# Optimization experiments

Hardware: AMD Instinct MI355X
Metric: run time of the kernel (lower is better)

The kernel has to match this reference:

```python
import jax, jax.numpy as jnp
import numpy as np

N = 16384          # number of feature-bank patches
D_IN = 1024        # raw feature dim
D_PROJ = 128       # projection dim (dimension_to_project_features_to)
PERCENTAGE = 0.01
NUM_SAMPLES = int(N * PERCENTAGE)  # 163 greedy coreset iterations


def setup_inputs() -> dict:
    key = jax.random.key(0)
    k1, k2 = jax.random.split(key)
    features = jax.random.normal(k1, (N, D_IN), dtype=jnp.float32)
    # random linear projection (torch.nn.Linear(D_IN, D_PROJ, bias=False))
    W = jax.random.normal(k2, (D_IN, D_PROJ), dtype=jnp.float32) / np.sqrt(D_IN)
    return {"features": features, "W": W}


def reference(features, W):
    # _reduce_features: random linear projection to D_PROJ
    reduced = features @ W  # [N, D_PROJ]

    # _compute_batchwise_differences: pairwise Euclidean distances [N, N]
    sq = jnp.sum(reduced * reduced, axis=1)  # [N]
    dist2 = sq[:, None] + sq[None, :] - 2.0 * (reduced @ reduced.T)
    dist = jnp.sqrt(jnp.clip(dist2, 0.0, None))  # [N, N]

    # initial anchor distances: torch.norm(distance_matrix, dim=1)
    anchor0 = jnp.sqrt(jnp.sum(dist * dist, axis=1))  # [N]

    # greedy farthest-point sampling loop (fused via scan)
    def step(anchor, _):
        select_idx = jnp.argmax(anchor)
        col = jax.lax.dynamic_index_in_dim(dist.T, select_idx, axis=0,
                                           keepdims=False)  # dist[:, idx]
        anchor = jnp.minimum(anchor, col)
        return anchor, select_idx

    _, coreset_indices = jax.lax.scan(step, anchor0, None, length=NUM_SAMPLES)

    # return subsampled feature bank [NUM_SAMPLES, D_IN]
    return features[coreset_indices]
```

## Files before the change

### kernel.cpp

```cpp
#include <hip/hip_runtime.h>

#define NPTS 16384
#define DIN  1024
#define DP   128
#define NS   163
#define NBLK 64
#define BTHR 256
#define WPB  (BTHR / 64)

__global__ __launch_bounds__(256) void k_proj(const float* __restrict__ F,
                                              const float* __restrict__ W,
                                              float* __restrict__ R) {
    __shared__ float As[32][36];
    __shared__ float Bs[32][128];
    const int tid = threadIdx.x;
    const int bm  = blockIdx.x;
    const int lr  = tid >> 3;
    const int lc  = (tid & 7) * 4;
    const int bkr = tid >> 5;
    const int bc  = (tid & 31) * 4;
    const int r0  = (tid >> 5) * 4;
    const int c0  = (tid & 31) * 4;

    float acc[4][4] = {};

    for (int k0 = 0; k0 < DIN; k0 += 32) {
        __syncthreads();
        *(float4*)&As[lr][lc] =
            *(const float4*)&F[(size_t)(bm * 32 + lr) * DIN + k0 + lc];
        #pragma unroll
        for (int p = 0; p < 4; ++p) {
            const int kk = bkr + p * 8;
            *(float4*)&Bs[kk][bc] = *(const float4*)&W[(size_t)(k0 + kk) * DP + bc];
        }
        __syncthreads();
        #pragma unroll
        for (int kt = 0; kt < 32; kt += 4) {
            float4 a[4], b[4];
            #pragma unroll
            for (int i = 0; i < 4; ++i) a[i] = *(const float4*)&As[r0 + i][kt];
            #pragma unroll
            for (int j = 0; j < 4; ++j) b[j] = *(const float4*)&Bs[kt + j][c0];
            #pragma unroll
            for (int i = 0; i < 4; ++i) {
                acc[i][0] += a[i].x * b[0].x; acc[i][1] += a[i].x * b[0].y;
                acc[i][2] += a[i].x * b[0].z; acc[i][3] += a[i].x * b[0].w;
                acc[i][0] += a[i].y * b[1].x; acc[i][1] += a[i].y * b[1].y;
                acc[i][2] += a[i].y * b[1].z; acc[i][3] += a[i].y * b[1].w;
                acc[i][0] += a[i].z * b[2].x; acc[i][1] += a[i].z * b[2].y;
                acc[i][2] += a[i].z * b[2].z; acc[i][3] += a[i].z * b[2].w;
                acc[i][0] += a[i].w * b[3].x; acc[i][1] += a[i].w * b[3].y;
                acc[i][2] += a[i].w * b[3].z; acc[i][3] += a[i].w * b[3].w;
            }
        }
    }
    #pragma unroll
    for (int i = 0; i < 4; ++i) {
        float4 v = make_float4(acc[i][0], acc[i][1], acc[i][2], acc[i][3]);
        *(float4*)&R[(size_t)(bm * 32 + r0 + i) * DP + c0] = v;
    }
}

__global__ void k_sq(const float* __restrict__ R, float* __restrict__ sq) {
    const int lane = threadIdx.x & 63;
    const int wave = (blockIdx.x * blockDim.x + threadIdx.x) >> 6;
    for (int row = wave; row < NPTS; row += 256) {
        const float a = R[(size_t)row * DP + lane];
        const float b = R[(size_t)row * DP + 64 + lane];
        float v = a * a + b * b;
        #pragma unroll
        for (int off = 32; off; off >>= 1) v += __shfl_xor(v, off);
        if (lane == 0) sq[row] = v;
    }
}

__global__ __launch_bounds__(256) void k_colpart(const float* __restrict__ R,
                                                 const float* __restrict__ sq,
                                                 float* __restrict__ part,
                                                 float* __restrict__ part_sq,
                                                 unsigned long long* __restrict__ gmax) {
    const int b = blockIdx.x, tid = threadIdx.x;

    const int slot = b * 256 + tid;
    if (slot < NS * NBLK) gmax[slot] = 0ull;

    if (tid < DP) {
        float acc = 0.0f;
        const float* p = R + (size_t)b * 256 * DP + tid;
        #pragma unroll 8
        for (int r = 0; r < 256; ++r) acc += p[(size_t)r * DP];
        part[b * DP + tid] = acc;
    } else if (tid < 192) {
        const int lane = tid - 128;
        const float* s = sq + b * 256;
        float v = s[lane] + s[64 + lane] + s[128 + lane] + s[192 + lane];
        #pragma unroll
        for (int off = 32; off; off >>= 1) v += __shfl_xor(v, off);
        if (lane == 0) part_sq[b] = v;
    }
}

__global__ void k_colfin(const float* __restrict__ part, const float* __restrict__ part_sq,
                         float* __restrict__ tS) {
    const int tid = threadIdx.x;
    if (tid < DP) {
        float acc = 0.0f;
        #pragma unroll 8
        for (int b = 0; b < 64; ++b) acc += part[b * DP + tid];
        tS[tid] = acc;
    } else if (tid == DP) {
        float s = 0.0f;
        #pragma unroll
        for (int b = 0; b < 64; ++b) s += part_sq[b];
        tS[DP] = s;
    }
}

__global__ __launch_bounds__(BTHR, 1) void k_greedy(
    const float* __restrict__ R, const float* __restrict__ sq,
    const float* __restrict__ tS, const float* __restrict__ F,
    unsigned long long* gmax, float* __restrict__ out) {
    __shared__ unsigned long long lmax[WPB];
    __shared__ unsigned sidx_cur;
    __shared__ unsigned sidx[(NS + NBLK - 1) / NBLK];

    const int tid  = threadIdx.x;
    const int lane = tid & 63;
    const int wid  = tid >> 6;
    const int bid  = blockIdx.x;
    const int g    = bid * BTHR + tid;

    float4 rr[32];
    #pragma unroll
    for (int q = 0; q < 32; ++q) rr[q] = *(const float4*)&R[(size_t)g * DP + q * 4];
    const float sqi = sq[g];

    float a0 = 0.f, a1 = 0.f, a2 = 0.f, a3 = 0.f;
    #pragma unroll
    for (int q = 0; q < 32; ++q) {
        const float4 t4 = *(const float4*)&tS[q * 4];
        a0 += rr[q].x * t4.x; a1 += rr[q].y * t4.y;
        a2 += rr[q].z * t4.z; a3 += rr[q].w * t4.w;
    }
    const float S = tS[DP];
    float anchor = sqrtf(fmaxf((float)NPTS * sqi + S - 2.0f * ((a0 + a1) + (a2 + a3)), 0.0f));

    for (int k = 0; k < NS; ++k) {
        unsigned long long key =
            ((unsigned long long)__float_as_uint(anchor) << 32) |
            (unsigned long long)(0xFFFFFFFFu - (unsigned)g);
        #pragma unroll
        for (int off = 32; off; off >>= 1) {
            const unsigned long long o = __shfl_xor(key, off);
            key = (o > key) ? o : key;
        }
        if (lane == 0) lmax[wid] = key;
        __syncthreads();

        if (wid == 0) {
            if (lane == 0) {
                unsigned long long bk = lmax[0];
                #pragma unroll
                for (int w = 1; w < WPB; ++w) bk = (lmax[w] > bk) ? lmax[w] : bk;
                __hip_atomic_store(&gmax[(size_t)k * NBLK + bid], bk,
                                   __ATOMIC_RELAXED, __HIP_MEMORY_SCOPE_AGENT);
            }
            const unsigned long long* gs = &gmax[(size_t)k * NBLK];
            unsigned long long v =
                __hip_atomic_load(&gs[lane], __ATOMIC_RELAXED, __HIP_MEMORY_SCOPE_AGENT);
            while (!__all(v != 0ull)) {
                __builtin_amdgcn_s_sleep(2);
                v = __hip_atomic_load(&gs[lane], __ATOMIC_RELAXED, __HIP_MEMORY_SCOPE_AGENT);
            }
            #pragma unroll
            for (int off = 32; off; off >>= 1) {
                const unsigned long long o = __shfl_xor(v, off);
                v = (o > v) ? o : v;
            }
            if (lane == 0) {
                const unsigned idx = 0xFFFFFFFFu - (unsigned)(v & 0xFFFFFFFFull);
                sidx_cur = idx;
                if ((k & 63) == bid) sidx[k >> 6] = idx;
            }
        }
        __syncthreads();
        const unsigned idx = sidx_cur;

        const float sqs = sq[idx];
        const float* rs = &R[(size_t)idx * DP];
        float d0 = 0.f, d1 = 0.f, d2 = 0.f, d3 = 0.f;
        #pragma unroll
        for (int q = 0; q < 32; ++q) {
            const float4 w4 = *(const float4*)&rs[q * 4];
            d0 += rr[q].x * w4.x; d1 += rr[q].y * w4.y;
            d2 += rr[q].z * w4.z; d3 += rr[q].w * w4.w;
        }
        const float d = sqrtf(fmaxf(sqi + sqs - 2.0f * ((d0 + d1) + (d2 + d3)), 0.0f));
        anchor = fminf(anchor, d);

        #pragma unroll
        for (int q = 0; q < 32; ++q)
            asm volatile("" : "+v"(rr[q].x), "+v"(rr[q].y), "+v"(rr[q].z), "+v"(rr[q].w));
    }

    __syncthreads();
    #pragma unroll
    for (int q = 0; q < 3; ++q) {
        const int k = q * NBLK + bid;
        if (k < NS) {
            const unsigned idx = sidx[q];
            *(float4*)&out[(size_t)k * DIN + tid * 4] =
                *(const float4*)&F[(size_t)idx * DIN + tid * 4];
        }
    }
}

extern "C" void kernel_launch(void* const* d_in, const int* in_sizes, int n_in,
                              void* d_out, int out_size, void* d_ws, size_t ws_size,
                              hipStream_t stream) {
    const float* F = (const float*)d_in[0];
    const float* W = (const float*)d_in[1];
    float* out = (float*)d_out;

    float* R       = (float*)d_ws;
    float* sq      = R + (size_t)NPTS * DP;
    float* tS      = sq + NPTS;
    float* part    = tS + 132;
    float* part_sq = part + 64 * DP;
    unsigned long long* gmax = (unsigned long long*)(part_sq + 64);

    hipLaunchKernelGGL(k_proj, dim3(NPTS / 32), dim3(256), 0, stream, F, W, R);
    hipLaunchKernelGGL(k_sq, dim3(64), dim3(256), 0, stream, R, sq);
    hipLaunchKernelGGL(k_colpart, dim3(64), dim3(256), 0, stream, R, sq, part, part_sq, gmax);
    hipLaunchKernelGGL(k_colfin, dim3(1), dim3(256), 0, stream, part, part_sq, tS);

    const float* Rc = R; const float* sqc = sq; const float* tSc = tS; const float* Fc = F;
    unsigned long long* gm = gmax; float* op = out;
    void* args[] = { (void*)&Rc, (void*)&sqc, (void*)&tSc, (void*)&Fc,
                     (void*)&gm, (void*)&op };
    hipLaunchCooperativeKernel((const void*)k_greedy, dim3(NBLK), dim3(BTHR),
                               args, 0, stream);
}
```

Measured before the change: 731.1 us.

## Use single-wave blocks in greedy kernel to drop intra-block barriers

```diff
diff --git a/kernel.cpp b/kernel.cpp
--- a/kernel.cpp
+++ b/kernel.cpp
@@ -4,9 +4,8 @@
 #define DIN  1024
 #define DP   128
 #define NS   163
-#define NBLK 64
-#define BTHR 256
-#define WPB  (BTHR / 64)
+#define NBLK 256
+#define BTHR 64
 
 __global__ __launch_bounds__(256) void k_proj(const float* __restrict__ F,
                                               const float* __restrict__ W,
@@ -81,8 +80,7 @@
                                                  unsigned long long* __restrict__ gmax) {
     const int b = blockIdx.x, tid = threadIdx.x;
 
-    const int slot = b * 256 + tid;
-    if (slot < NS * NBLK) gmax[slot] = 0ull;
+    for (int s = b * 256 + tid; s < NS * NBLK; s += 64 * 256) gmax[s] = 0ull;
 
     if (tid < DP) {
         float acc = 0.0f;
@@ -120,15 +118,9 @@
     const float* __restrict__ R, const float* __restrict__ sq,
     const float* __restrict__ tS, const float* __restrict__ F,
     unsigned long long* gmax, float* __restrict__ out) {
-    __shared__ unsigned long long lmax[WPB];
-    __shared__ unsigned sidx_cur;
-    __shared__ unsigned sidx[(NS + NBLK - 1) / NBLK];
-
-    const int tid  = threadIdx.x;
-    const int lane = tid & 63;
-    const int wid  = tid >> 6;
-    const int bid  = blockIdx.x;
-    const int g    = bid * BTHR + tid;
+    const int tid = threadIdx.x;
+    const int bid = blockIdx.x;
+    const int g   = (bid << 6) | tid;
 
     float4 rr[32];
     #pragma unroll
@@ -145,6 +137,8 @@
     const float S = tS[DP];
     float anchor = sqrtf(fmaxf((float)NPTS * sqi + S - 2.0f * ((a0 + a1) + (a2 + a3)), 0.0f));
 
+    unsigned myidx = 0;
+
     for (int k = 0; k < NS; ++k) {
         unsigned long long key =
             ((unsigned long long)__float_as_uint(anchor) << 32) |
@@ -154,37 +148,35 @@
             const unsigned long long o = __shfl_xor(key, off);
             key = (o > key) ? o : key;
         }
-        if (lane == 0) lmax[wid] = key;
-        __syncthreads();
-
-        if (wid == 0) {
-            if (lane == 0) {
-                unsigned long long bk = lmax[0];
-                #pragma unroll
-                for (int w = 1; w < WPB; ++w) bk = (lmax[w] > bk) ? lmax[w] : bk;
-                __hip_atomic_store(&gmax[(size_t)k * NBLK + bid], bk,
-                                   __ATOMIC_RELAXED, __HIP_MEMORY_SCOPE_AGENT);
-            }
-            const unsigned long long* gs = &gmax[(size_t)k * NBLK];
-            unsigned long long v =
-                __hip_atomic_load(&gs[lane], __ATOMIC_RELAXED, __HIP_MEMORY_SCOPE_AGENT);
-            while (!__all(v != 0ull)) {
-                __builtin_amdgcn_s_sleep(2);
-                v = __hip_atomic_load(&gs[lane], __ATOMIC_RELAXED, __HIP_MEMORY_SCOPE_AGENT);
-            }
-            #pragma unroll
-            for (int off = 32; off; off >>= 1) {
-                const unsigned long long o = __shfl_xor(v, off);
-                v = (o > v) ? o : v;
-            }
-            if (lane == 0) {
-                const unsigned idx = 0xFFFFFFFFu - (unsigned)(v & 0xFFFFFFFFull);
-                sidx_cur = idx;
-                if ((k & 63) == bid) sidx[k >> 6] = idx;
-            }
-        }
-        __syncthreads();
-        const unsigned idx = sidx_cur;
+        if (tid == 0)
+            __hip_atomic_store(&gmax[(size_t)k * NBLK + bid], key,
+                               __ATOMIC_RELAXED, __HIP_MEMORY_SCOPE_AGENT);
+
+        const unsigned long long* gs = &gmax[(size_t)k * NBLK];
+        unsigned long long v0, v1, v2, v3;
+        v0 = __hip_atomic_load(&gs[tid      ], __ATOMIC_RELAXED, __HIP_MEMORY_SCOPE_AGENT);
+        v1 = __hip_atomic_load(&gs[tid +  64], __ATOMIC_RELAXED, __HIP_MEMORY_SCOPE_AGENT);
+        v2 = __hip_atomic_load(&gs[tid + 128], __ATOMIC_RELAXED, __HIP_MEMORY_SCOPE_AGENT);
+        v3 = __hip_atomic_load(&gs[tid + 192], __ATOMIC_RELAXED, __HIP_MEMORY_SCOPE_AGENT);
+        while (!__all((v0 != 0ull) & (v1 != 0ull) & (v2 != 0ull) & (v3 != 0ull))) {
+            __builtin_amdgcn_s_sleep(1);
+            v0 = __hip_atomic_load(&gs[tid      ], __ATOMIC_RELAXED, __HIP_MEMORY_SCOPE_AGENT);
+            v1 = __hip_atomic_load(&gs[tid +  64], __ATOMIC_RELAXED, __HIP_MEMORY_SCOPE_AGENT);
+            v2 = __hip_atomic_load(&gs[tid + 128], __ATOMIC_RELAXED, __HIP_MEMORY_SCOPE_AGENT);
+            v3 = __hip_atomic_load(&gs[tid + 192], __ATOMIC_RELAXED, __HIP_MEMORY_SCOPE_AGENT);
+        }
+
+        unsigned long long m = v0;
+        if (v1 > m) m = v1;
+        if (v2 > m) m = v2;
+        if (v3 > m) m = v3;
+        #pragma unroll
+        for (int off = 32; off; off >>= 1) {
+            const unsigned long long o = __shfl_xor(m, off);
+            m = (o > m) ? o : m;
+        }
+        const unsigned idx = 0xFFFFFFFFu - (unsigned)(m & 0xFFFFFFFFull);
+        if (k == bid) myidx = idx;
 
         const float sqs = sq[idx];
         const float* rs = &R[(size_t)idx * DP];
@@ -203,14 +195,12 @@
             asm volatile("" : "+v"(rr[q].x), "+v"(rr[q].y), "+v"(rr[q].z), "+v"(rr[q].w));
     }
 
-    __syncthreads();
-    #pragma unroll
-    for (int q = 0; q < 3; ++q) {
-        const int k = q * NBLK + bid;
-        if (k < NS) {
-            const unsigned idx = sidx[q];
-            *(float4*)&out[(size_t)k * DIN + tid * 4] =
-                *(const float4*)&F[(size_t)idx * DIN + tid * 4];
+    if (bid < NS) {
+        #pragma unroll
+        for (int p = 0; p < DIN / (BTHR * 4); ++p) {
+            const int c = (p * BTHR + tid) * 4;
+            *(float4*)&out[(size_t)bid * DIN + c] =
+                *(const float4*)&F[(size_t)myidx * DIN + c];
         }
     }
 }
```

New measurement: 951.1 us, median of 4. 1.3x slower.

## Select multiple greedy coreset points per global sync using top-4 candidate speculation

Applied to the files above, without the earlier changes.

```diff
diff --git a/kernel.cpp b/kernel.cpp
--- a/kernel.cpp
+++ b/kernel.cpp
@@ -7,6 +7,10 @@
 #define NBLK 64
 #define BTHR 256
 #define WPB  (BTHR / 64)
+#define CMARGIN 1e-3f
+
+typedef unsigned long long u64;
+typedef unsigned int u32;
 
 __global__ __launch_bounds__(256) void k_proj(const float* __restrict__ F,
                                               const float* __restrict__ W,
@@ -78,11 +82,11 @@
                                                  const float* __restrict__ sq,
                                                  float* __restrict__ part,
                                                  float* __restrict__ part_sq,
-                                                 unsigned long long* __restrict__ gmax) {
+                                                 u64* __restrict__ gmax) {
     const int b = blockIdx.x, tid = threadIdx.x;
-
-    const int slot = b * 256 + tid;
-    if (slot < NS * NBLK) gmax[slot] = 0ull;
+    const int gt = b * 256 + tid;
+
+    for (int s = gt; s < NS * NBLK * 4; s += 64 * 256) gmax[s] = 0ull;
 
     if (tid < DP) {
         float acc = 0.0f;
@@ -116,13 +120,29 @@
     }
 }
 
+__device__ __forceinline__ u64 wavemax_u64(u64 k) {
+    #pragma unroll
+    for (int off = 32; off; off >>= 1) {
+        const u64 o = __shfl_xor(k, off);
+        k = (o > k) ? o : k;
+    }
+    return k;
+}
+
+__device__ __forceinline__ float wsum_f32(float v) {
+    #pragma unroll
+    for (int off = 32; off; off >>= 1) v += __shfl_xor(v, off);
+    return v;
+}
+
 __global__ __launch_bounds__(BTHR, 1) void k_greedy(
     const float* __restrict__ R, const float* __restrict__ sq,
     const float* __restrict__ tS, const float* __restrict__ F,
-    unsigned long long* gmax, float* __restrict__ out) {
-    __shared__ unsigned long long lmax[WPB];
-    __shared__ unsigned sidx_cur;
-    __shared__ unsigned sidx[(NS + NBLK - 1) / NBLK];
+    u64* gmax, float* __restrict__ out) {
+    __shared__ u64 lmax[WPB][4];
+    __shared__ u32 bc_idx[4];
+    __shared__ u32 bc_cnt;
+    __shared__ u32 sidx[(NS + NBLK - 1) / NBLK];
 
     const int tid  = threadIdx.x;
     const int lane = tid & 63;
@@ -145,58 +165,145 @@
     const float S = tS[DP];
     float anchor = sqrtf(fmaxf((float)NPTS * sqi + S - 2.0f * ((a0 + a1) + (a2 + a3)), 0.0f));
 
-    for (int k = 0; k < NS; ++k) {
-        unsigned long long key =
-            ((unsigned long long)__float_as_uint(anchor) << 32) |
-            (unsigned long long)(0xFFFFFFFFu - (unsigned)g);
-        #pragma unroll
-        for (int off = 32; off; off >>= 1) {
-            const unsigned long long o = __shfl_xor(key, off);
-            key = (o > key) ? o : key;
-        }
-        if (lane == 0) lmax[wid] = key;
+    int nsel = 0, r = 0;
+
+    while (nsel < NS) {
+        const u64 key =
+            ((u64)__float_as_uint(anchor) << 32) |
+            (u64)(0xFFFFFFFFu - (unsigned)g);
+        u64 kx = key;
+        const u64 k1 = wavemax_u64(kx); kx = (kx == k1) ? 0ull : kx;
+        const u64 k2 = wavemax_u64(kx); kx = (kx == k2) ? 0ull : kx;
+        const u64 k3 = wavemax_u64(kx); kx = (kx == k3) ? 0ull : kx;
+        const u64 k4 = wavemax_u64(kx);
+        if (lane == 0) { lmax[wid][0] = k1; lmax[wid][1] = k2; lmax[wid][2] = k3; lmax[wid][3] = k4; }
         __syncthreads();
 
         if (wid == 0) {
             if (lane == 0) {
-                unsigned long long bk = lmax[0];
+                u64 t0 = 0, t1 = 0, t2 = 0, t3 = 0;
                 #pragma unroll
-                for (int w = 1; w < WPB; ++w) bk = (lmax[w] > bk) ? lmax[w] : bk;
-                __hip_atomic_store(&gmax[(size_t)k * NBLK + bid], bk,
-                                   __ATOMIC_RELAXED, __HIP_MEMORY_SCOPE_AGENT);
-            }
-            const unsigned long long* gs = &gmax[(size_t)k * NBLK];
-            unsigned long long v =
-                __hip_atomic_load(&gs[lane], __ATOMIC_RELAXED, __HIP_MEMORY_SCOPE_AGENT);
-            while (!__all(v != 0ull)) {
+                for (int w = 0; w < WPB; ++w) {
+                    #pragma unroll
+                    for (int j = 0; j < 4; ++j) {
+                        const u64 v = lmax[w][j];
+                        if (v > t0)      { t3 = t2; t2 = t1; t1 = t0; t0 = v; }
+                        else if (v > t1) { t3 = t2; t2 = t1; t1 = v; }
+                        else if (v > t2) { t3 = t2; t2 = v; }
+                        else if (v > t3) { t3 = v; }
+                    }
+                }
+                u64* dst = &gmax[((size_t)r * NBLK + bid) * 4];
+                __hip_atomic_store(&dst[0], t0, __ATOMIC_RELAXED, __HIP_MEMORY_SCOPE_AGENT);
+                __hip_atomic_store(&dst[1], t1, __ATOMIC_RELAXED, __HIP_MEMORY_SCOPE_AGENT);
+                __hip_atomic_store(&dst[2], t2, __ATOMIC_RELAXED, __HIP_MEMORY_SCOPE_AGENT);
+                __hip_atomic_store(&dst[3], t3, __ATOMIC_RELAXED, __HIP_MEMORY_SCOPE_AGENT);
+            }
+            const u64* gs = &gmax[(size_t)r * NBLK * 4];
+            u64 v0, v1, v2, v3;
+            v0 = __hip_atomic_load(&gs[lane      ], __ATOMIC_RELAXED, __HIP_MEMORY_SCOPE_AGENT);
+            v1 = __hip_atomic_load(&gs[lane +  64], __ATOMIC_RELAXED, __HIP_MEMORY_SCOPE_AGENT);
+            v2 = __hip_atomic_load(&gs[lane + 128], __ATOMIC_RELAXED, __HIP_MEMORY_SCOPE_AGENT);
+            v3 = __hip_atomic_load(&gs[lane + 192], __ATOMIC_RELAXED, __HIP_MEMORY_SCOPE_AGENT);
+            while (!__all((v0 != 0ull) & (v1 != 0ull) & (v2 != 0ull) & (v3 != 0ull))) {
                 __builtin_amdgcn_s_sleep(2);
-                v = __hip_atomic_load(&gs[lane], __ATOMIC_RELAXED, __HIP_MEMORY_SCOPE_AGENT);
-            }
-            #pragma unroll
-            for (int off = 32; off; off >>= 1) {
-                const unsigned long long o = __shfl_xor(v, off);
-                v = (o > v) ? o : v;
+                v0 = __hip_atomic_load(&gs[lane      ], __ATOMIC_RELAXED, __HIP_MEMORY_SCOPE_AGENT);
+                v1 = __hip_atomic_load(&gs[lane +  64], __ATOMIC_RELAXED, __HIP_MEMORY_SCOPE_AGENT);
+                v2 = __hip_atomic_load(&gs[lane + 128], __ATOMIC_RELAXED, __HIP_MEMORY_SCOPE_AGENT);
+                v3 = __hip_atomic_load(&gs[lane + 192], __ATOMIC_RELAXED, __HIP_MEMORY_SCOPE_AGENT);
+            }
+
+            u64 vm = v0; if (v1 > vm) vm = v1; if (v2 > vm) vm = v2; if (v3 > vm) vm = v3;
+            const u64 b4 = wavemax_u64(((lane & 3) == 3) ? vm : 0ull);
+
+            u64 w0 = v0, w1 = v1, w2 = v2, w3 = v3;
+            u64 e0, e1, e2, e3, e4;
+            {
+                u64 m;
+                #define GTOP(EOUT)                                            \
+                    m = w0; if (w1 > m) m = w1; if (w2 > m) m = w2;           \
+                    if (w3 > m) m = w3; m = wavemax_u64(m); EOUT = m;         \
+                    w0 = (w0 == m) ? 0ull : w0; w1 = (w1 == m) ? 0ull : w1;   \
+                    w2 = (w2 == m) ? 0ull : w2; w3 = (w3 == m) ? 0ull : w3;
+                GTOP(e0) GTOP(e1) GTOP(e2) GTOP(e3) GTOP(e4)
+                #undef GTOP
+            }
+            const u64 Uk  = (e4 > b4) ? e4 : b4;
+            const float Uf = __uint_as_float((u32)(Uk >> 32));
+
+            const u32 ci0 = 0xFFFFFFFFu - (u32)(e0 & 0xFFFFFFFFull);
+            const u32 ci1 = 0xFFFFFFFFu - (u32)(e1 & 0xFFFFFFFFull);
+            const u32 ci2 = 0xFFFFFFFFu - (u32)(e2 & 0xFFFFFFFFull);
+            const u32 ci3 = 0xFFFFFFFFu - (u32)(e3 & 0xFFFFFFFFull);
+            const float ca1 = __uint_as_float((u32)(e1 >> 32));
+            const float ca2 = __uint_as_float((u32)(e2 >> 32));
+            const float ca3 = __uint_as_float((u32)(e3 >> 32));
+            const float2 f0 = *(const float2*)&R[(size_t)ci0 * DP + 2 * lane];
+            const float2 f1 = *(const float2*)&R[(size_t)ci1 * DP + 2 * lane];
+            const float2 f2 = *(const float2*)&R[(size_t)ci2 * DP + 2 * lane];
+            const float2 f3 = *(const float2*)&R[(size_t)ci3 * DP + 2 * lane];
+            const float s0 = sq[ci0], s1 = sq[ci1], s2 = sq[ci2], s3 = sq[ci3];
+
+            const float p01 = wsum_f32(f0.x * f1.x + f0.y * f1.y);
+            const float p02 = wsum_f32(f0.x * f2.x + f0.y * f2.y);
+            const float p03 = wsum_f32(f0.x * f3.x + f0.y * f3.y);
+            const float p12 = wsum_f32(f1.x * f2.x + f1.y * f2.y);
+            const float p13 = wsum_f32(f1.x * f3.x + f1.y * f3.y);
+            const float p23 = wsum_f32(f2.x * f3.x + f2.y * f3.y);
+            const float d01 = sqrtf(fmaxf(s0 + s1 - 2.0f * p01, 0.0f));
+            const float d02 = sqrtf(fmaxf(s0 + s2 - 2.0f * p02, 0.0f));
+            const float d03 = sqrtf(fmaxf(s0 + s3 - 2.0f * p03, 0.0f));
+            const float d12 = sqrtf(fmaxf(s1 + s2 - 2.0f * p12, 0.0f));
+            const float d13 = sqrtf(fmaxf(s1 + s3 - 2.0f * p13, 0.0f));
+            const float d23 = sqrtf(fmaxf(s2 + s3 - 2.0f * p23, 0.0f));
+
+            float u1 = fminf(ca1, d01), u2 = fminf(ca2, d02), u3 = fminf(ca3, d03);
+            bool  l1 = true, l2 = true, l3 = true;
+            u32 o1 = 0, o2 = 0, o3 = 0;
+            int cnt = 1;
+            #pragma unroll
+            for (int step = 0; step < 3; ++step) {
+                if (nsel + cnt >= NS) break;
+                int jb = 0; float bf = -1.0f; u32 bidx = 0;
+                if (l1 && (u1 > bf || (u1 == bf && ci1 < bidx))) { bf = u1; bidx = ci1; jb = 1; }
+                if (l2 && (u2 > bf || (u2 == bf && ci2 < bidx))) { bf = u2; bidx = ci2; jb = 2; }
+                if (l3 && (u3 > bf || (u3 == bf && ci3 < bidx))) { bf = u3; bidx = ci3; jb = 3; }
+                if (jb == 0 || !(bf > Uf + CMARGIN)) break;
+                if (cnt == 1) o1 = bidx; else if (cnt == 2) o2 = bidx; else o3 = bidx;
+                ++cnt;
+                if (jb == 1)      { l1 = false; u2 = fminf(u2, d12); u3 = fminf(u3, d13); }
+                else if (jb == 2) { l2 = false; u1 = fminf(u1, d12); u3 = fminf(u3, d23); }
+                else              { l3 = false; u1 = fminf(u1, d13); u2 = fminf(u2, d23); }
             }
             if (lane == 0) {
-                const unsigned idx = 0xFFFFFFFFu - (unsigned)(v & 0xFFFFFFFFull);
-                sidx_cur = idx;
-                if ((k & 63) == bid) sidx[k >> 6] = idx;
+                bc_idx[0] = ci0;
+                if (cnt > 1) bc_idx[1] = o1;
+                if (cnt > 2) bc_idx[2] = o2;
+                if (cnt > 3) bc_idx[3] = o3;
+                bc_cnt = (u32)cnt;
             }
         }
         __syncthreads();
-        const unsigned idx = sidx_cur;
-
-        const float sqs = sq[idx];
-        const float* rs = &R[(size_t)idx * DP];
-        float d0 = 0.f, d1 = 0.f, d2 = 0.f, d3 = 0.f;
-        #pragma unroll
-        for (int q = 0; q < 32; ++q) {
-            const float4 w4 = *(const float4*)&rs[q * 4];
-            d0 += rr[q].x * w4.x; d1 += rr[q].y * w4.y;
-            d2 += rr[q].z * w4.z; d3 += rr[q].w * w4.w;
-        }
-        const float d = sqrtf(fmaxf(sqi + sqs - 2.0f * ((d0 + d1) + (d2 + d3)), 0.0f));
-        anchor = fminf(anchor, d);
+        const int cnt = (int)bc_cnt;
+
+        for (int c = 0; c < cnt; ++c) {
+            const u32 idx = bc_idx[c];
+            const int kk = nsel + c;
+            if (tid == 0 && (kk & 63) == bid) sidx[kk >> 6] = idx;
+            const float sqs = sq[idx];
+            const float* rs = &R[(size_t)idx * DP];
+            float d0 = 0.f, d1 = 0.f, d2 = 0.f, d3 = 0.f;
+            #pragma unroll
+            for (int q = 0; q < 32; ++q) {
+                const float4 w4 = *(const float4*)&rs[q * 4];
+                d0 += rr[q].x * w4.x; d1 += rr[q].y * w4.y;
+                d2 += rr[q].z * w4.z; d3 += rr[q].w * w4.w;
+            }
+            const float d = sqrtf(fmaxf(sqi + sqs - 2.0f * ((d0 + d1) + (d2 + d3)), 0.0f));
+            anchor = fminf(anchor, d);
+        }
+        nsel += cnt;
+        ++r;
 
         #pragma unroll
         for (int q = 0; q < 32; ++q)
@@ -227,7 +334,7 @@
     float* tS      = sq + NPTS;
     float* part    = tS + 132;
     float* part_sq = part + 64 * DP;
-    unsigned long long* gmax = (unsigned long long*)(part_sq + 64);
+    u64*   gmax    = (u64*)(part_sq + 64);
 
     hipLaunchKernelGGL(k_proj, dim3(NPTS / 32), dim3(256), 0, stream, F, W, R);
     hipLaunchKernelGGL(k_sq, dim3(64), dim3(256), 0, stream, R, sq);
@@ -235,7 +342,7 @@
     hipLaunchKernelGGL(k_colfin, dim3(1), dim3(256), 0, stream, part, part_sq, tS);
 
     const float* Rc = R; const float* sqc = sq; const float* tSc = tS; const float* Fc = F;
-    unsigned long long* gm = gmax; float* op = out;
+    u64* gm = gmax; float* op = out;
     void* args[] = { (void*)&Rc, (void*)&sqc, (void*)&tSc, (void*)&Fc,
                      (void*)&gm, (void*)&op };
     hipLaunchCooperativeKernel((const void*)k_greedy, dim3(NBLK), dim3(BTHR),
```

Result: faster. 594.5 us (-18.7%).
